# Kernel optimization log

Hardware: AMD Instinct MI355X
Metric: run time of the kernel (lower is better)

## Reference

```python
import math
import jax, jax.numpy as jnp
import numpy as np

B, N, D = 4, 4096, 1024
H = 16
DK = D // H  # 64
M = 256      # nb_features
EPS = 1e-6


def _gorf(key, n_rows, n_cols):
    """Gaussian orthogonal random matrix (n_rows, n_cols), stacked orthonormal
    blocks with chi-distributed row lengths (Performer GORF)."""
    blocks, rows_left = [], n_rows
    while rows_left > 0:
        br = min(n_cols, rows_left)
        key, k1, k2 = jax.random.split(key, 3)
        u = jax.random.normal(k1, (n_cols, n_cols), dtype=jnp.float32)
        q, r = jnp.linalg.qr(u)
        q = q * jnp.sign(jnp.diagonal(r))[None, :]  # q @ diag(sign(diag(r)))
        g = jax.random.normal(k2, (br, n_cols), dtype=jnp.float32)
        lengths = jnp.linalg.norm(g, axis=1, keepdims=True)
        blocks.append(q[:br] * lengths)
        rows_left -= br
    return jnp.concatenate(blocks, axis=0)


def setup_inputs() -> dict:
    key = jax.random.key(0)
    ks = jax.random.split(key, 8)
    x = jax.random.normal(ks[0], (B, N, D), dtype=jnp.float32)
    # True = PAD
    key_padding_mask = jax.random.randint(ks[1], (B, N), 0, 2).astype(jnp.bool_)
    # Linear params (xavier-scale init; exact scheme irrelevant to the math)
    Wqkv = jax.random.normal(ks[2], (3 * D, D), dtype=jnp.float32) * 0.02
    bqkv = jnp.zeros((3 * D,), dtype=jnp.float32)
    Wout = jax.random.normal(ks[3], (D, D), dtype=jnp.float32) * 0.02
    bout = jnp.zeros((D,), dtype=jnp.float32)
    # Per-head GORF omega, scaled by sqrt(dk) as in _draw_features
    omega = jnp.stack(
        [_gorf(jax.random.fold_in(ks[4], h), M, DK) for h in range(H)], axis=0
    ) * math.sqrt(DK)  # (H, M, dk)
    return {"x": x, "key_padding_mask": key_padding_mask, "Wqkv": Wqkv,
            "bqkv": bqkv, "Wout": Wout, "bout": bout, "omega": omega}


def _phi_exp(t, omega):
    # t: (B,H,N,dk) -> (B,H,N,M)
    proj = jnp.einsum('bhnd,hmd->bhnm', t, omega)
    sq_norm = 0.5 * jnp.sum(t * t, axis=-1, keepdims=True)
    z = proj - sq_norm
    z = z - jnp.max(z, axis=-1, keepdims=True)          # stabilize
    return jnp.exp(z) / math.sqrt(M + 1e-6)


def reference(x, key_padding_mask, Wqkv, bqkv, Wout, bout, omega):
    qkv = x @ Wqkv.T + bqkv                              # (B,N,3D)
    Q, K, V = jnp.split(qkv, 3, axis=-1)
    split = lambda t: t.reshape(B, N, H, DK).transpose(0, 2, 1, 3)  # (B,H,N,dk)
    Q, K, V = split(Q), split(K), split(V)
    valid_bool = ~key_padding_mask                       # (B,N), True=real token
    valid = valid_bool[:, None, :, None].astype(x.dtype) # (B,1,N,1)
    Qp = _phi_exp(Q, omega)                              # (B,H,N,M)
    Kp = _phi_exp(K, omega) * valid                      # zero PAD keys
    KV = jnp.einsum('bhnm,bhnd->bhmd', Kp, V)            # (B,H,M,dk)
    ksum = jnp.sum(Kp, axis=2)                           # (B,H,M)
    num = jnp.einsum('bhnm,bhmd->bhnd', Qp, KV)          # (B,H,N,dk)
    den = jnp.einsum('bhnm,bhm->bhn', Qp, ksum)[..., None] + EPS
    ctx = num / den                                      # (B,H,N,dk)
    out = ctx.transpose(0, 2, 1, 3).reshape(B, N, D)     # merge heads
    out = out @ Wout.T + bout
    out = out * valid_bool[..., None].astype(out.dtype)  # PAD queries -> exact 0
    return out
```

## Files before the change

### kernel.cpp

```cpp
#include <hip/hip_runtime.h>
#include <hip/hip_bf16.h>
#include <math.h>

#define B_  4
#define N_  4096
#define D_  1024
#define H_  16
#define DK_ 64
#define M_  256
#define R_  (B_*N_)
#define EPS_ 1e-6f
#define VTROWS_ 80
#define KVROWS_ 128
#define PHK_PAD 68
#define PHQ_PAD 264

typedef __bf16 bf16;
typedef __bf16 bf16x4 __attribute__((ext_vector_type(4)));
typedef __bf16 bf16x8 __attribute__((ext_vector_type(8)));
typedef _Float16 f16;
typedef _Float16 f16x4 __attribute__((ext_vector_type(4)));
typedef _Float16 f16x8 __attribute__((ext_vector_type(8)));
typedef float  f32x4  __attribute__((ext_vector_type(4)));

#define GLD(gp, lp) __builtin_amdgcn_global_load_lds( \
    (const __attribute__((address_space(1))) void*)(gp), \
    (__attribute__((address_space(3))) void*)(lp), 16, 0, 0)

#define BAR_()   __builtin_amdgcn_s_barrier()
#define SBAR_()  __builtin_amdgcn_sched_barrier(0)
#define PRIO1_() __builtin_amdgcn_s_setprio(1)
#define PRIO0_() __builtin_amdgcn_s_setprio(0)

__global__ __launch_bounds__(256)
void split_f16v(const float* __restrict__ in, f16* __restrict__ hi,
                f16* __restrict__ lo, int n4)
{
    int i = blockIdx.x * 256 + threadIdx.x;
    if (i < n4) {
        float4 v = ((const float4*)in)[i];
        f16x4 h = { (f16)v.x, (f16)v.y, (f16)v.z, (f16)v.w };
        ((f16x4*)hi)[i] = h;
        if (lo) {
            f16x4 l = { (f16)(v.x - (float)h[0]), (f16)(v.y - (float)h[1]),
                        (f16)(v.z - (float)h[2]), (f16)(v.w - (float)h[3]) };
            ((f16x4*)lo)[i] = l;
        }
    }
}

__global__ __launch_bounds__(256)
void f32_to_bf16v(const float* __restrict__ in, bf16* __restrict__ o, int n4)
{
    int i = blockIdx.x * 256 + threadIdx.x;
    if (i < n4) {
        float4 v = ((const float4*)in)[i];
        bf16x4 h = { (bf16)v.x, (bf16)v.y, (bf16)v.z, (bf16)v.w };
        ((bf16x4*)o)[i] = h;
    }
}

__global__ __launch_bounds__(256)
void zero_f32(float* __restrict__ p, int n)
{
    int i = blockIdx.x * 256 + threadIdx.x;
    if (i < n) p[i] = 0.f;
}

__global__ __launch_bounds__(256)
void init_vt(bf16* __restrict__ VT)
{
    int i = blockIdx.x * 256 + threadIdx.x;
    if (i >= B_*H_*16*N_) return;
    int bh  = i >> 16;
    int rem = i & 65535;
    int row = 64 + (rem >> 12);
    int n   = rem & (N_-1);
    VT[((size_t)bh*VTROWS_ + row)*N_ + n] = (row == 64) ? (bf16)1.0f : (bf16)0.0f;
}

__global__ __launch_bounds__(256)
void pack_kv(const float* __restrict__ KVt32, bf16* __restrict__ KVb)
{
    int i = blockIdx.x * 256 + threadIdx.x;
    if (i >= B_*H_*KVROWS_*M_) return;
    int bh  = i >> 15;
    int rem = i & 32767;
    int row = rem >> 8;
    int m   = rem & (M_-1);
    bf16 o = (bf16)0.0f;
    if (row < 64) {
        o = (bf16)KVt32[((size_t)bh*VTROWS_ + row)*M_ + m];
    } else if (row == 64) {
        o = (bf16)KVt32[((size_t)bh*VTROWS_ + 64)*M_ + m];
    } else if (row == 65) {
        float v = KVt32[((size_t)bh*VTROWS_ + 64)*M_ + m];
        o = (bf16)(v - (float)(bf16)v);
    }
    KVb[i] = o;
}


#define STAGE_(dstbuf, srcp, kt, half) do { \
    _Pragma("unroll") \
    for (int q_ = 0; q_ < 2; ++q_) { \
        int idx_ = q_*512 + tid; \
        int row_ = idx_ >> 3; \
        int seg_ = (idx_ & 7) ^ (row_ & 7); \
        GLD((srcp) + (size_t)((half)*128 + row_) * D_ + (kt)*64 + seg_*8, \
            &(dstbuf)[(half)*8192 + idx_*8]); \
    } } while (0)

#define LDA_(buf, i0) do { \
    _Pragma("unroll") \
    for (int i_ = 0; i_ < 4; ++i_) { \
        _Pragma("unroll") \
        for (int k_ = 0; k_ < 2; ++k_) { \
            int row_ = warp_m*128 + ((i0)+i_)*16 + m16; \
            int off_ = (row_*128 + k_*64 + quad*16) ^ ((row_ & 7) << 4); \
            a[i_][k_] = *(const f16x8*)((const char*)(buf) + off_); \
        } } } while (0)

#define LDB_(buf, j0) do { \
    _Pragma("unroll") \
    for (int j_ = 0; j_ < 2; ++j_) { \
        _Pragma("unroll") \
        for (int k_ = 0; k_ < 2; ++k_) { \
            int row_ = warp_n*64 + ((j0)+j_)*16 + m16; \
            int off_ = (row_*128 + k_*64 + quad*16) ^ ((row_ & 7) << 4); \
            b[(j0)+j_][k_] = *(const f16x8*)((const char*)(buf) + off_); \
        } } } while (0)

#define MFMA_Q(I0, J0) do { \
    _Pragma("unroll") \
    for (int i_ = 0; i_ < 4; ++i_) { \
        _Pragma("unroll") \
        for (int j_ = 0; j_ < 2; ++j_) { \
            _Pragma("unroll") \
            for (int k_ = 0; k_ < 2; ++k_) \
                acc[(I0)+i_][(J0)+j_] = __builtin_amdgcn_mfma_f32_16x16x32_f16( \
                    a[i_][k_], b[(J0)+j_][k_], acc[(I0)+i_][(J0)+j_], 0, 0, 0); \
        } } } while (0)

#define LGK0_()  do { asm volatile("s_waitcnt lgkmcnt(0)"); SBAR_(); } while (0)
#define LGK8_()  asm volatile("s_waitcnt lgkmcnt(8)")
#define VMC4_()  do { asm volatile("s_waitcnt vmcnt(4)"); SBAR_(); } while (0)

__global__ __launch_bounds__(512, 1)
void gemm_qkv(const f16* __restrict__ X, const f16* __restrict__ Wh,
              const float* __restrict__ bqkv,
              f16* __restrict__ Qh, f16* __restrict__ Kh, bf16* __restrict__ VT)
{
    __shared__ __align__(16) f16 sA[2][256*64];
    __shared__ __align__(16) f16 sB[2][256*64];
    const int tid = threadIdx.x;

    const int nwg  = gridDim.x * gridDim.y;
    int flat = blockIdx.y * gridDim.x + blockIdx.x;
    int wgid = (flat & 7) * (nwg >> 3) + (flat >> 3);
    const int bm = (wgid / 12) * 256;
    const int bn = (wgid % 12) * 256;

    const int lane = tid & 63, wave = tid >> 6;
    const int warp_m = wave >> 2, warp_n = wave & 3;
    const int m16 = lane & 15, quad = lane >> 4;

    const f16* gA = X  + (size_t)bm * D_;
    const f16* gB = Wh + (size_t)bn * D_;

    f32x4 acc[8][4];
    #pragma unroll
    for (int i = 0; i < 8; ++i)
        #pragma unroll
        for (int j = 0; j < 4; ++j)
            acc[i][j] = (f32x4){0.f, 0.f, 0.f, 0.f};

    f16x8 a[4][2], b[4][2];

    STAGE_(sA[0], gA, 0, 0);
    STAGE_(sA[0], gA, 0, 1);
    STAGE_(sB[0], gB, 0, 0);
    STAGE_(sB[0], gB, 0, 1);
    STAGE_(sB[1], gB, 1, 0);
    STAGE_(sB[1], gB, 1, 1);
    VMC4_();
    BAR_();

    for (int it = 0; it < 8; ++it) {
        const int t1 = 2*it + 1, t2 = 2*it + 2, t3 = 2*it + 3;
        LDA_(sA[0], 0); LDB_(sB[0], 0);
        STAGE_(sA[1], gA, t1, 0);
        LGK8_();
        BAR_(); LGK0_();
        PRIO1_(); MFMA_Q(0, 0); PRIO0_();
        BAR_();

        LDB_(sB[0], 2);
        STAGE_(sA[1], gA, t1, 1);
        BAR_(); LGK0_();
        PRIO1_(); MFMA_Q(0, 2); PRIO0_();
        BAR_();

        LDA_(sA[0], 4);
        if (t2 < 16) STAGE_(sB[0], gB, t2, 0);
        BAR_(); LGK0_();
        PRIO1_(); MFMA_Q(4, 2); PRIO0_();
        BAR_();

        if (t2 < 16) STAGE_(sB[0], gB, t2, 1);
        VMC4_();
        BAR_();
        PRIO1_(); MFMA_Q(4, 0); PRIO0_();
        BAR_();

        LDA_(sA[1], 0); LDB_(sB[1], 0);
        if (t2 < 16) STAGE_(sA[0], gA, t2, 0);
        LGK8_();
        BAR_(); LGK0_();
        PRIO1_(); MFMA_Q(0, 0); PRIO0_();
        BAR_();

        LDB_(sB[1], 2);
        if (t2 < 16) STAGE_(sA[0], gA, t2, 1);
        BAR_(); LGK0_();
        PRIO1_(); MFMA_Q(0, 2); PRIO0_();
        BAR_();

        LDA_(sA[1], 4);
        if (t3 < 16) STAGE_(sB[1], gB, t3, 0);
        BAR_(); LGK0_();
        PRIO1_(); MFMA_Q(4, 2); PRIO0_();
        BAR_();

        if (t3 < 16) STAGE_(sB[1], gB, t3, 1);
        VMC4_();
        BAR_();
        PRIO1_(); MFMA_Q(4, 0); PRIO0_();
        BAR_();
    }

    #pragma unroll
    for (int j = 0; j < 4; ++j) {
        int gcol = bn + warp_n*64 + j*16 + m16;
        float bv = bqkv[gcol];
        #pragma unroll
        for (int i = 0; i < 8; ++i) {
            int row0 = bm + warp_m*128 + i*16 + quad*4;
            if (gcol >= 2*D_) {
                int vcol = gcol - 2*D_;
                int hh = vcol >> 6, dd = vcol & 63;
                int bb = row0 >> 12, nn = row0 & (N_-1);
                bf16x4 pk = { (bf16)(acc[i][j][0]+bv), (bf16)(acc[i][j][1]+bv),
                              (bf16)(acc[i][j][2]+bv), (bf16)(acc[i][j][3]+bv) };
                *(bf16x4*)&VT[(((size_t)bb*H_+hh)*VTROWS_ + dd)*N_ + nn] = pk;
            } else if (gcol >= D_) {
                #pragma unroll
                for (int r = 0; r < 4; ++r)
                    Kh[(size_t)(row0+r) * D_ + gcol - D_] = (f16)(acc[i][j][r] + bv);
            } else {
                #pragma unroll
                for (int r = 0; r < 4; ++r)
                    Qh[(size_t)(row0+r) * D_ + gcol] = (f16)(acc[i][j][r] + bv);
            }
        }
    }
}

#define STAGEK_(sub_, bi_) do { \
    const int n0_ = nsp*1024 + (sub_)*128; \
    _Pragma("unroll") \
    for (int it_ = 0; it_ < 2; ++it_) { \
        int idx_ = it_*512 + tid; \
        int row_ = idx_ >> 3, seg_ = (idx_ & 7) ^ (row_ & 7); \
        GLD(Kh + (size_t)(b*N_ + n0_ + row_) * D_ + h*DK_ + seg_*8, \
            &sK[bi_][idx_*8]); \
    } } while (0)

#define STAGEVT_(sub_) do { \
    const int n0_ = nsp*1024 + (sub_)*128; \
    _Pragma("unroll") \
    for (int it_ = 0; it_ < 2; ++it_) { \
        int idx_ = it_*512 + tid; \
        int row_ = idx_ >> 4, seg_ = (idx_ & 15) ^ (row_ & 7); \
        GLD(VT + ((size_t)bh*VTROWS_ + row_)*N_ + n0_ + seg_*8, \
            &sVT[idx_*8]); \
    } \
    if (tid < 256) { \
        int idx_ = 1024 + tid; \
        int row_ = idx_ >> 4, seg_ = (idx_ & 15) ^ (row_ & 7); \
        GLD(VT + ((size_t)bh*VTROWS_ + row_)*N_ + n0_ + seg_*8, \
            &sVT[idx_*8]); \
    } } while (0)

#define STAGEOM_(arr_, src_) do { \
    _Pragma("unroll") \
    for (int q_ = 0; q_ < 4; ++q_) { \
        int idx_ = q_*512 + tid; \
        int row_ = idx_ >> 3, seg_ = (idx_ & 7) ^ (row_ & 7); \
        GLD((src_) + (size_t)row_*DK_ + seg_*8, &(arr_)[idx_*8]); \
    } } while (0)

__global__ __launch_bounds__(512, 1)
void fused_kv(const f16* __restrict__ Kh, const bf16* __restrict__ VT,
              const f16* __restrict__ omhi, const f16* __restrict__ omlo,
              const int* __restrict__ mask, float* __restrict__ KVt32)
{
    __shared__ __align__(16) f16  sK[2][128*64];
    __shared__ __align__(16) bf16 sVT[VTROWS_*128];
    __shared__ __align__(16) f16  sOmH[M_*DK_];
    __shared__ __align__(16) f16  sOmL[M_*DK_];
    __shared__ __align__(16) bf16 sPhi[M_*PHK_PAD];
    const int nsp = blockIdx.x;
    const int h = blockIdx.y, b = blockIdx.z;
    const int bh = b*H_ + h;
    const int tid = threadIdx.x, lane = tid & 63, wave = tid >> 6;
    const int m16 = lane & 15, quad = lane >> 4;
    const int wm = wave * 32;
    const int nloc = wave*16 + quad*4;
    const float inv_sqrt_m = rsqrtf((float)M_ + 1e-6f);
    const f16* omh = omhi + (size_t)h * M_ * DK_;
    const f16* oml = omlo + (size_t)h * M_ * DK_;

    f32x4 kvacc[5][2];
    #pragma unroll
    for (int d = 0; d < 5; ++d)
        #pragma unroll
        for (int j = 0; j < 2; ++j)
            kvacc[d][j] = (f32x4){0.f, 0.f, 0.f, 0.f};

    STAGEOM_(sOmH, omh);
    STAGEOM_(sOmL, oml);
    STAGEK_(0, 0);

    for (int sub = 0; sub < 8; ++sub) {
        const int cur = sub & 1;
        const int n0 = nsp*1024 + sub*128;

        asm volatile("s_waitcnt vmcnt(0) lgkmcnt(0)");
        SBAR_();
        BAR_();

        int4 mv4 = *(const int4*)&mask[b*N_ + n0 + nloc];
        const int* mv = (const int*)&mv4;
        STAGEVT_(sub);
        if (sub < 7) STAGEK_(sub+1, cur^1);

        const char* kb = (const char*)&sK[cur][0];
        const int rowb = wave*16 + m16;
        f16x8 ah0 = *(const f16x8*)(kb + ((rowb*128 +      quad*16) ^ ((rowb & 7) << 4)));
        f16x8 ah1 = *(const f16x8*)(kb + ((rowb*128 + 64 + quad*16) ^ ((rowb & 7) << 4)));

        f32x4 acc[16];
        #pragma unroll
        for (int j = 0; j < 16; ++j) acc[j] = (f32x4){0.f, 0.f, 0.f, 0.f};

        PRIO1_();
        #pragma unroll
        for (int j = 0; j < 16; ++j) {
            int rowm = j*16 + m16;
            int bo0 = (rowm*128 +      quad*16) ^ ((rowm & 7) << 4);
            int bo1 = (rowm*128 + 64 + quad*16) ^ ((rowm & 7) << 4);
            f16x8 bh0 = *(const f16x8*)((const char*)sOmH + bo0);
            f16x8 bh1 = *(const f16x8*)((const char*)sOmH + bo1);
            f16x8 bl0 = *(const f16x8*)((const char*)sOmL + bo0);
            f16x8 bl1 = *(const f16x8*)((const char*)sOmL + bo1);
            acc[j] = __builtin_amdgcn_mfma_f32_16x16x32_f16(ah0, bh0, acc[j], 0,0,0);
            acc[j] = __builtin_amdgcn_mfma_f32_16x16x32_f16(ah0, bl0, acc[j], 0,0,0);
            acc[j] = __builtin_amdgcn_mfma_f32_16x16x32_f16(ah1, bh1, acc[j], 0,0,0);
            acc[j] = __builtin_amdgcn_mfma_f32_16x16x32_f16(ah1, bl1, acc[j], 0,0,0);
        }
        PRIO0_();

        #pragma unroll
        for (int r = 0; r < 4; ++r) {
            float mx = acc[0][r];
            #pragma unroll
            for (int j = 1; j < 16; ++j) mx = fmaxf(mx, acc[j][r]);
            mx = fmaxf(mx, __shfl_xor(mx, 1, 64));
            mx = fmaxf(mx, __shfl_xor(mx, 2, 64));
            mx = fmaxf(mx, __shfl_xor(mx, 4, 64));
            mx = fmaxf(mx, __shfl_xor(mx, 8, 64));
            #pragma unroll
            for (int j = 0; j < 16; ++j)
                acc[j][r] = __expf(acc[j][r] - mx) * inv_sqrt_m;
        }

        if (wave < 4) {
            #pragma unroll
            for (int j = 0; j < 16; ++j) {
                bf16x4 pk;
                #pragma unroll
                for (int r = 0; r < 4; ++r)
                    pk[r] = mv[r] ? (bf16)0.0f : (bf16)acc[j][r];
                *(bf16x4*)&sPhi[(j*16 + m16)*PHK_PAD + nloc] = pk;
            }
        }
        asm volatile("s_waitcnt lgkmcnt(0)");
        if (sub < 7) { asm volatile("s_waitcnt vmcnt(2)"); }
        else         { asm volatile("s_waitcnt vmcnt(0)"); }
        SBAR_();
        BAR_();

        PRIO1_();
        #pragma unroll
        for (int ks = 0; ks < 2; ++ks) {
            bf16x8 av[5], bp[2];
            #pragma unroll
            for (int d = 0; d < 5; ++d) {
                int rowv = d*16 + m16;
                av[d] = *(const bf16x8*)((const char*)sVT +
                        ((rowv*256 + ks*64 + quad*16) ^ ((rowv & 7) << 4)));
            }
            #pragma unroll
            for (int j = 0; j < 2; ++j)
                bp[j] = *(const bf16x8*)&sPhi[(wm + j*16 + m16)*PHK_PAD + ks*32 + quad*8];
            #pragma unroll
            for (int d = 0; d < 5; ++d)
                #pragma unroll
                for (int j = 0; j < 2; ++j)
                    kvacc[d][j] = __builtin_amdgcn_mfma_f32_16x16x32_bf16(
                        av[d], bp[j], kvacc[d][j], 0, 0, 0);
        }
        PRIO0_();
        asm volatile("s_waitcnt lgkmcnt(0)");
        SBAR_();
        BAR_();

        if (wave >= 4) {
            #pragma unroll
            for (int j = 0; j < 16; ++j) {
                bf16x4 pk;
                #pragma unroll
                for (int r = 0; r < 4; ++r)
                    pk[r] = mv[r] ? (bf16)0.0f : (bf16)acc[j][r];
                *(bf16x4*)&sPhi[(j*16 + m16)*PHK_PAD + (nloc - 64)] = pk;
            }
        }
        asm volatile("s_waitcnt lgkmcnt(0)");
        SBAR_();
        BAR_();

        PRIO1_();
        #pragma unroll
        for (int ks = 0; ks < 2; ++ks) {
            bf16x8 av[5], bp[2];
            #pragma unroll
            for (int d = 0; d < 5; ++d) {
                int rowv = d*16 + m16;
                av[d] = *(const bf16x8*)((const char*)sVT +
                        ((rowv*256 + 128 + ks*64 + quad*16) ^ ((rowv & 7) << 4)));
            }
            #pragma unroll
            for (int j = 0; j < 2; ++j)
                bp[j] = *(const bf16x8*)&sPhi[(wm + j*16 + m16)*PHK_PAD + ks*32 + quad*8];
            #pragma unroll
            for (int d = 0; d < 5; ++d)
                #pragma unroll
                for (int j = 0; j < 2; ++j)
                    kvacc[d][j] = __builtin_amdgcn_mfma_f32_16x16x32_bf16(
                        av[d], bp[j], kvacc[d][j], 0, 0, 0);
        }
        PRIO0_();
    }

    #pragma unroll
    for (int d = 0; d < 5; ++d)
        #pragma unroll
        for (int j = 0; j < 2; ++j) {
            int drow = d*16 + quad*4;
            int m = wm + j*16 + m16;
            #pragma unroll
            for (int r = 0; r < 4; ++r)
                atomicAdd(&KVt32[((size_t)bh*VTROWS_ + drow + r)*M_ + m],
                          kvacc[d][j][r]);
        }
}

__global__ __launch_bounds__(512, 1)
void fused_ctx(const f16* __restrict__ Qh, const f16* __restrict__ omhi,
               const f16* __restrict__ omlo, const bf16* __restrict__ KVb,
               bf16* __restrict__ ctx)
{
    __shared__ __align__(16) f16  sOmH[M_*DK_];
    __shared__ __align__(16) f16  sOmL[M_*DK_];
    __shared__ __align__(16) bf16 sPhi[128*PHQ_PAD];
    __shared__ float sden[2][128];
    const int nsp = blockIdx.x;
    const int h = blockIdx.y, b = blockIdx.z;
    const int bh = b*H_ + h;
    const int tid = threadIdx.x, lane = tid & 63, wave = tid >> 6;
    const int m16 = lane & 15, quad = lane >> 4;
    const float inv_sqrt_m = rsqrtf((float)M_ + 1e-6f);
    const f16* omh = omhi + (size_t)h * M_ * DK_;
    const f16* oml = omlo + (size_t)h * M_ * DK_;

    STAGEOM_(sOmH, omh);
    STAGEOM_(sOmL, oml);
    asm volatile("s_waitcnt vmcnt(0)");
    SBAR_();
    BAR_();

    const int wq = wave >> 2;
    const int wc = wave & 3;

    for (int nb = 0; nb < 8; ++nb) {
        const int q0 = nsp*1024 + nb*128;

        const int rowq = wave*16 + m16;
        f16x8 ah0 = *(const f16x8*)&Qh[(size_t)(b*N_ + q0 + rowq)*D_ + h*DK_ + quad*8];
        f16x8 ah1 = *(const f16x8*)&Qh[(size_t)(b*N_ + q0 + rowq)*D_ + h*DK_ + 32 + quad*8];

        f32x4 acc[16];
        #pragma unroll
        for (int j = 0; j < 16; ++j) acc[j] = (f32x4){0.f, 0.f, 0.f, 0.f};

        PRIO1_();
        #pragma unroll
        for (int j = 0; j < 16; ++j) {
            int rowm = j*16 + m16;
            int bo0 = (rowm*128 +      quad*16) ^ ((rowm & 7) << 4);
            int bo1 = (rowm*128 + 64 + quad*16) ^ ((rowm & 7) << 4);
            f16x8 bh0 = *(const f16x8*)((const char*)sOmH + bo0);
            f16x8 bh1 = *(const f16x8*)((const char*)sOmH + bo1);
            f16x8 bl0 = *(const f16x8*)((const char*)sOmL + bo0);
            f16x8 bl1 = *(const f16x8*)((const char*)sOmL + bo1);
            acc[j] = __builtin_amdgcn_mfma_f32_16x16x32_f16(ah0, bh0, acc[j], 0,0,0);
            acc[j] = __builtin_amdgcn_mfma_f32_16x16x32_f16(ah0, bl0, acc[j], 0,0,0);
            acc[j] = __builtin_amdgcn_mfma_f32_16x16x32_f16(ah1, bh1, acc[j], 0,0,0);
            acc[j] = __builtin_amdgcn_mfma_f32_16x16x32_f16(ah1, bl1, acc[j], 0,0,0);
        }
        PRIO0_();

        bf16x8 wf[2][8];
        #pragma unroll
        for (int jr = 0; jr < 2; ++jr) {
            int rowk = wc*32 + jr*16 + m16;
            #pragma unroll
            for (int ks = 0; ks < 8; ++ks)
                wf[jr][ks] = *(const bf16x8*)&KVb[((size_t)bh*KVROWS_ + rowk)*M_
                                                  + ks*32 + quad*8];
        }

        #pragma unroll
        for (int r = 0; r < 4; ++r) {
            float mx = acc[0][r];
            #pragma unroll
            for (int j = 1; j < 16; ++j) mx = fmaxf(mx, acc[j][r]);
            mx = fmaxf(mx, __shfl_xor(mx, 1, 64));
            mx = fmaxf(mx, __shfl_xor(mx, 2, 64));
            mx = fmaxf(mx, __shfl_xor(mx, 4, 64));
            mx = fmaxf(mx, __shfl_xor(mx, 8, 64));
            #pragma unroll
            for (int j = 0; j < 16; ++j)
                acc[j][r] = __expf(acc[j][r] - mx) * inv_sqrt_m;
        }

        {
            int nloc0 = wave*16 + quad*4;
            #pragma unroll
            for (int j = 0; j < 16; ++j)
                #pragma unroll
                for (int r = 0; r < 4; ++r)
                    sPhi[(nloc0 + r)*PHQ_PAD + j*16 + m16] = (bf16)acc[j][r];
        }
        asm volatile("s_waitcnt lgkmcnt(0)");
        SBAR_();
        BAR_();

        f32x4 cacc[4][2];
        #pragma unroll
        for (int i = 0; i < 4; ++i)
            #pragma unroll
            for (int j = 0; j < 2; ++j)
                cacc[i][j] = (f32x4){0.f, 0.f, 0.f, 0.f};

        PRIO1_();
        #pragma unroll
        for (int ks = 0; ks < 8; ++ks) {
            bf16x8 af[4];
            #pragma unroll
            for (int i = 0; i < 4; ++i)
                af[i] = *(const bf16x8*)&sPhi[(wq*64 + i*16 + m16)*PHQ_PAD
                                              + ks*32 + quad*8];
            #pragma unroll
            for (int i = 0; i < 4; ++i)
                #pragma unroll
                for (int jr = 0; jr < 2; ++jr)
                    cacc[i][jr] = __builtin_amdgcn_mfma_f32_16x16x32_bf16(
                        af[i], wf[jr][ks], cacc[i][jr], 0, 0, 0);
        }
        PRIO0_();

        if (wc == 2 && m16 < 2) {
            #pragma unroll
            for (int i = 0; i < 4; ++i)
                #pragma unroll
                for (int r = 0; r < 4; ++r)
                    sden[m16][wq*64 + i*16 + quad*4 + r] = cacc[i][0][r];
        }
        asm volatile("s_waitcnt lgkmcnt(0)");
        SBAR_();
        BAR_();

        if (wc < 2) {
            #pragma unroll
            for (int i = 0; i < 4; ++i) {
                #pragma unroll
                for (int r = 0; r < 4; ++r) {
                    int lrow = wq*64 + i*16 + quad*4 + r;
                    float den = sden[0][lrow] + sden[1][lrow] + EPS_;
                    #pragma unroll
                    for (int jr = 0; jr < 2; ++jr)
                        ctx[(size_t)(b*N_ + q0 + lrow)*D_ + h*DK_
                            + wc*32 + jr*16 + m16] = (bf16)(cacc[i][jr][r] / den);
                }
            }
        }
        asm volatile("s_waitcnt lgkmcnt(0)");
        SBAR_();
        BAR_();
    }
}

__global__ __launch_bounds__(256)
void gemm_out(const bf16* __restrict__ A, const bf16* __restrict__ W,
              const float* __restrict__ bias, float* __restrict__ C,
              const int* __restrict__ mask)
{
    __shared__ bf16 sA[128*64];
    __shared__ bf16 sB[128*64];
    const int tid  = threadIdx.x;
    const int bm   = blockIdx.y * 128;
    const int bn   = blockIdx.x * 128;
    const int lane = tid & 63, wave = tid >> 6;
    const int wm   = (wave & 1) * 64, wn = (wave >> 1) * 64;
    const int m16  = lane & 15, quad = lane >> 4;

    f32x4 acc[4][4];
    #pragma unroll
    for (int i = 0; i < 4; ++i)
        #pragma unroll
        for (int j = 0; j < 4; ++j)
            acc[i][j] = (f32x4){0.f, 0.f, 0.f, 0.f};

    for (int k0 = 0; k0 < D_; k0 += 64) {
        __syncthreads();
        #pragma unroll
        for (int it = 0; it < 4; ++it) {
            int idx = it*256 + tid;
            int row = idx >> 3, seg = idx & 7;
            GLD(A + (size_t)(bm + row) * D_ + k0 + seg*8, &sA[idx*8]);
            GLD(W + (size_t)(bn + row) * D_ + k0 + seg*8, &sB[idx*8]);
        }
        __syncthreads();
        #pragma unroll
        for (int kk = 0; kk < 64; kk += 32) {
            bf16x8 af[4], bfr[4];
            #pragma unroll
            for (int i = 0; i < 4; ++i)
                af[i] = *(const bf16x8*)&sA[(wm + i*16 + m16)*64 + kk + quad*8];
            #pragma unroll
            for (int j = 0; j < 4; ++j)
                bfr[j] = *(const bf16x8*)&sB[(wn + j*16 + m16)*64 + kk + quad*8];
            #pragma unroll
            for (int i = 0; i < 4; ++i)
                #pragma unroll
                for (int j = 0; j < 4; ++j)
                    acc[i][j] = __builtin_amdgcn_mfma_f32_16x16x32_bf16(
                        af[i], bfr[j], acc[i][j], 0, 0, 0);
        }
    }

    #pragma unroll
    for (int j = 0; j < 4; ++j) {
        int col = bn + wn + j*16 + m16;
        float bv = bias[col];
        #pragma unroll
        for (int i = 0; i < 4; ++i) {
            int row0 = bm + wm + i*16 + quad*4;
            #pragma unroll
            for (int r = 0; r < 4; ++r) {
                int row = row0 + r;
                float v = acc[i][j][r] + bv;
                if (mask[row] != 0) v = 0.0f;
                C[(size_t)row * D_ + col] = v;
            }
        }
    }
}

extern "C" void kernel_launch(void* const* d_in, const int* in_sizes, int n_in,
                              void* d_out, int out_size, void* d_ws, size_t ws_size,
                              hipStream_t stream)
{
    const float* x     = (const float*)d_in[0];
    const int*   mask  = (const int*)d_in[1];
    const float* Wqkv  = (const float*)d_in[2];
    const float* bqkv  = (const float*)d_in[3];
    const float* Wout  = (const float*)d_in[4];
    const float* bout  = (const float*)d_in[5];
    const float* omega = (const float*)d_in[6];
    float* out = (float*)d_out;

    char* w = (char*)d_ws;
    f16*   Wh    = (f16*)w;    w += (size_t)3*D_*D_ * 2;
    bf16*  Wob   = (bf16*)w;   w += (size_t)D_*D_ * 2;
    f16*   omhi  = (f16*)w;    w += (size_t)H_*M_*DK_ * 2;
    f16*   omlo  = (f16*)w;    w += (size_t)H_*M_*DK_ * 2;
    f16*   xh    = (f16*)w;    w += (size_t)R_ * D_ * 2;
    f16*   Qh    = (f16*)w;    w += (size_t)R_ * D_ * 2;
    f16*   Kh    = (f16*)w;    w += (size_t)R_ * D_ * 2;
    bf16*  VT    = (bf16*)w;   w += (size_t)B_*H_*VTROWS_*N_ * 2;
    float* KVt32 = (float*)w;  w += (size_t)B_*H_*VTROWS_*M_ * 4;
    bf16*  KVb   = (bf16*)w;   w += (size_t)B_*H_*KVROWS_*M_ * 2;
    bf16*  VC    = (bf16*)Kh;

    split_f16v<<<(R_*D_/4 + 255)/256, 256, 0, stream>>>(x, xh, nullptr, R_*D_/4);
    split_f16v<<<(3*D_*D_/4 + 255)/256, 256, 0, stream>>>(Wqkv, Wh, nullptr, 3*D_*D_/4);
    split_f16v<<<(H_*M_*DK_/4 + 255)/256, 256, 0, stream>>>(omega, omhi, omlo, H_*M_*DK_/4);
    f32_to_bf16v<<<(D_*D_/4 + 255)/256, 256, 0, stream>>>(Wout, Wob, D_*D_/4);
    zero_f32<<<(B_*H_*VTROWS_*M_ + 255)/256, 256, 0, stream>>>(KVt32, B_*H_*VTROWS_*M_);
    init_vt<<<(B_*H_*16*N_ + 255)/256, 256, 0, stream>>>(VT);

    gemm_qkv<<<dim3(3*D_/256, R_/256), 512, 0, stream>>>(xh, Wh, bqkv, Qh, Kh, VT);

    fused_kv<<<dim3(4, H_, B_), 512, 0, stream>>>(Kh, VT, omhi, omlo, mask, KVt32);

    pack_kv<<<(B_*H_*KVROWS_*M_ + 255)/256, 256, 0, stream>>>(KVt32, KVb);

    fused_ctx<<<dim3(4, H_, B_), 512, 0, stream>>>(Qh, omhi, omlo, KVb, VC);

    gemm_out<<<dim3(8, R_/128), 256, 0, stream>>>(VC, Wob, bout, out, mask);
}
```

Baseline: 457.5 us.

## Split QKV GEMM into QK and V kernels; reuse pipelined 256x256 GEMM for output projection

The fused QKV GEMM is split into two kernels. The Q/K kernel swaps the MFMA operands so each lane holds four consecutive columns and writes vectorized f16x4 row-major stores instead of scalar stores. The V kernel keeps the transposed bf16 layout. The output projection moves from a simple 128x128 single-buffered kernel to the same 8-phase double-buffered 256x256 pipeline with vectorized float4 stores. The cost is one more launch and a smaller output grid (256 blocks), which may leave some compute units idle.

```diff
diff --git a/kernel.cpp b/kernel.cpp
--- a/kernel.cpp
+++ b/kernel.cpp
@@ -31,6 +31,9 @@
 #define SBAR_()  __builtin_amdgcn_sched_barrier(0)
 #define PRIO1_() __builtin_amdgcn_s_setprio(1)
 #define PRIO0_() __builtin_amdgcn_s_setprio(0)
+#define LGK0_()  do { asm volatile("s_waitcnt lgkmcnt(0)"); SBAR_(); } while (0)
+#define LGK8_()  asm volatile("s_waitcnt lgkmcnt(8)")
+#define VMC4_()  do { asm volatile("s_waitcnt vmcnt(4)"); SBAR_(); } while (0)
 
 __global__ __launch_bounds__(256)
 void split_f16v(const float* __restrict__ in, f16* __restrict__ hi,
@@ -100,7 +103,6 @@
     KVb[i] = o;
 }
 
-
 #define STAGE_(dstbuf, srcp, kt, half) do { \
     _Pragma("unroll") \
     for (int q_ = 0; q_ < 2; ++q_) { \
@@ -111,55 +113,129 @@
             &(dstbuf)[(half)*8192 + idx_*8]); \
     } } while (0)
 
-#define LDA_(buf, i0) do { \
+#define LDA_G(T, buf, i0) do { \
     _Pragma("unroll") \
     for (int i_ = 0; i_ < 4; ++i_) { \
         _Pragma("unroll") \
         for (int k_ = 0; k_ < 2; ++k_) { \
             int row_ = warp_m*128 + ((i0)+i_)*16 + m16; \
             int off_ = (row_*128 + k_*64 + quad*16) ^ ((row_ & 7) << 4); \
-            a[i_][k_] = *(const f16x8*)((const char*)(buf) + off_); \
+            a[i_][k_] = *(const T*)((const char*)(buf) + off_); \
         } } } while (0)
 
-#define LDB_(buf, j0) do { \
+#define LDB_G(T, buf, j0) do { \
     _Pragma("unroll") \
     for (int j_ = 0; j_ < 2; ++j_) { \
         _Pragma("unroll") \
         for (int k_ = 0; k_ < 2; ++k_) { \
             int row_ = warp_n*64 + ((j0)+j_)*16 + m16; \
             int off_ = (row_*128 + k_*64 + quad*16) ^ ((row_ & 7) << 4); \
-            b[(j0)+j_][k_] = *(const f16x8*)((const char*)(buf) + off_); \
+            b[(j0)+j_][k_] = *(const T*)((const char*)(buf) + off_); \
         } } } while (0)
 
-#define MFMA_Q(I0, J0) do { \
-    _Pragma("unroll") \
-    for (int i_ = 0; i_ < 4; ++i_) { \
+#define MFMA_F16N(I0, J0) do { \
+    _Pragma("unroll") \
+    for (int i_ = 0; i_ < 4; ++i_) \
         _Pragma("unroll") \
-        for (int j_ = 0; j_ < 2; ++j_) { \
+        for (int j_ = 0; j_ < 2; ++j_) \
             _Pragma("unroll") \
             for (int k_ = 0; k_ < 2; ++k_) \
                 acc[(I0)+i_][(J0)+j_] = __builtin_amdgcn_mfma_f32_16x16x32_f16( \
                     a[i_][k_], b[(J0)+j_][k_], acc[(I0)+i_][(J0)+j_], 0, 0, 0); \
-        } } } while (0)
-
-#define LGK0_()  do { asm volatile("s_waitcnt lgkmcnt(0)"); SBAR_(); } while (0)
-#define LGK8_()  asm volatile("s_waitcnt lgkmcnt(8)")
-#define VMC4_()  do { asm volatile("s_waitcnt vmcnt(4)"); SBAR_(); } while (0)
-
-__global__ __launch_bounds__(512, 1)
-void gemm_qkv(const f16* __restrict__ X, const f16* __restrict__ Wh,
-              const float* __restrict__ bqkv,
-              f16* __restrict__ Qh, f16* __restrict__ Kh, bf16* __restrict__ VT)
+    } while (0)
+
+#define MFMA_F16S(I0, J0) do { \
+    _Pragma("unroll") \
+    for (int i_ = 0; i_ < 4; ++i_) \
+        _Pragma("unroll") \
+        for (int j_ = 0; j_ < 2; ++j_) \
+            _Pragma("unroll") \
+            for (int k_ = 0; k_ < 2; ++k_) \
+                acc[(I0)+i_][(J0)+j_] = __builtin_amdgcn_mfma_f32_16x16x32_f16( \
+                    b[(J0)+j_][k_], a[i_][k_], acc[(I0)+i_][(J0)+j_], 0, 0, 0); \
+    } while (0)
+
+#define MFMA_BF16S(I0, J0) do { \
+    _Pragma("unroll") \
+    for (int i_ = 0; i_ < 4; ++i_) \
+        _Pragma("unroll") \
+        for (int j_ = 0; j_ < 2; ++j_) \
+            _Pragma("unroll") \
+            for (int k_ = 0; k_ < 2; ++k_) \
+                acc[(I0)+i_][(J0)+j_] = __builtin_amdgcn_mfma_f32_16x16x32_bf16( \
+                    b[(J0)+j_][k_], a[i_][k_], acc[(I0)+i_][(J0)+j_], 0, 0, 0); \
+    } while (0)
+
+#define KLOOP_8PH(MFMA_OP) \
+    STAGE_(sA[0], gA, 0, 0); \
+    STAGE_(sA[0], gA, 0, 1); \
+    STAGE_(sB[0], gB, 0, 0); \
+    STAGE_(sB[0], gB, 0, 1); \
+    STAGE_(sB[1], gB, 1, 0); \
+    STAGE_(sB[1], gB, 1, 1); \
+    VMC4_(); \
+    BAR_(); \
+    for (int it = 0; it < 8; ++it) { \
+        const int t1 = 2*it + 1, t2 = 2*it + 2, t3 = 2*it + 3; \
+        LDA_G(FRAG_T, sA[0], 0); LDB_G(FRAG_T, sB[0], 0); \
+        STAGE_(sA[1], gA, t1, 0); \
+        LGK8_(); \
+        BAR_(); LGK0_(); \
+        PRIO1_(); MFMA_OP(0, 0); PRIO0_(); \
+        BAR_(); \
+        LDB_G(FRAG_T, sB[0], 2); \
+        STAGE_(sA[1], gA, t1, 1); \
+        BAR_(); LGK0_(); \
+        PRIO1_(); MFMA_OP(0, 2); PRIO0_(); \
+        BAR_(); \
+        LDA_G(FRAG_T, sA[0], 4); \
+        if (t2 < 16) STAGE_(sB[0], gB, t2, 0); \
+        BAR_(); LGK0_(); \
+        PRIO1_(); MFMA_OP(4, 2); PRIO0_(); \
+        BAR_(); \
+        if (t2 < 16) STAGE_(sB[0], gB, t2, 1); \
+        VMC4_(); \
+        BAR_(); \
+        PRIO1_(); MFMA_OP(4, 0); PRIO0_(); \
+        BAR_(); \
+        LDA_G(FRAG_T, sA[1], 0); LDB_G(FRAG_T, sB[1], 0); \
+        if (t2 < 16) STAGE_(sA[0], gA, t2, 0); \
+        LGK8_(); \
+        BAR_(); LGK0_(); \
+        PRIO1_(); MFMA_OP(0, 0); PRIO0_(); \
+        BAR_(); \
+        LDB_G(FRAG_T, sB[1], 2); \
+        if (t2 < 16) STAGE_(sA[0], gA, t2, 1); \
+        BAR_(); LGK0_(); \
+        PRIO1_(); MFMA_OP(0, 2); PRIO0_(); \
+        BAR_(); \
+        LDA_G(FRAG_T, sA[1], 4); \
+        if (t3 < 16) STAGE_(sB[1], gB, t3, 0); \
+        BAR_(); LGK0_(); \
+        PRIO1_(); MFMA_OP(4, 2); PRIO0_(); \
+        BAR_(); \
+        if (t3 < 16) STAGE_(sB[1], gB, t3, 1); \
+        VMC4_(); \
+        BAR_(); \
+        PRIO1_(); MFMA_OP(4, 0); PRIO0_(); \
+        BAR_(); \
+    }
+
+#define FRAG_T f16x8
+__global__ __launch_bounds__(512)
+void gemm_qkv_qk(const f16* __restrict__ X, const f16* __restrict__ Wh,
+                 const float* __restrict__ bqkv,
+                 f16* __restrict__ Qh, f16* __restrict__ Kh)
 {
     __shared__ __align__(16) f16 sA[2][256*64];
     __shared__ __align__(16) f16 sB[2][256*64];
     const int tid = threadIdx.x;
 
-    const int nwg  = gridDim.x * gridDim.y;
+    const int nwg = gridDim.x * gridDim.y;
     int flat = blockIdx.y * gridDim.x + blockIdx.x;
     int wgid = (flat & 7) * (nwg >> 3) + (flat >> 3);
-    const int bm = (wgid / 12) * 256;
-    const int bn = (wgid % 12) * 256;
+    const int bm = (wgid >> 3) * 256;
+    const int bn = (wgid & 7) * 256;
 
     const int lane = tid & 63, wave = tid >> 6;
     const int warp_m = wave >> 2, warp_n = wave & 3;
@@ -174,97 +250,128 @@
         #pragma unroll
         for (int j = 0; j < 4; ++j)
             acc[i][j] = (f32x4){0.f, 0.f, 0.f, 0.f};
-
     f16x8 a[4][2], b[4][2];
 
-    STAGE_(sA[0], gA, 0, 0);
-    STAGE_(sA[0], gA, 0, 1);
-    STAGE_(sB[0], gB, 0, 0);
-    STAGE_(sB[0], gB, 0, 1);
-    STAGE_(sB[1], gB, 1, 0);
-    STAGE_(sB[1], gB, 1, 1);
-    VMC4_();
-    BAR_();
-
-    for (int it = 0; it < 8; ++it) {
-        const int t1 = 2*it + 1, t2 = 2*it + 2, t3 = 2*it + 3;
-        LDA_(sA[0], 0); LDB_(sB[0], 0);
-        STAGE_(sA[1], gA, t1, 0);
-        LGK8_();
-        BAR_(); LGK0_();
-        PRIO1_(); MFMA_Q(0, 0); PRIO0_();
-        BAR_();
-
-        LDB_(sB[0], 2);
-        STAGE_(sA[1], gA, t1, 1);
-        BAR_(); LGK0_();
-        PRIO1_(); MFMA_Q(0, 2); PRIO0_();
-        BAR_();
-
-        LDA_(sA[0], 4);
-        if (t2 < 16) STAGE_(sB[0], gB, t2, 0);
-        BAR_(); LGK0_();
-        PRIO1_(); MFMA_Q(4, 2); PRIO0_();
-        BAR_();
-
-        if (t2 < 16) STAGE_(sB[0], gB, t2, 1);
-        VMC4_();
-        BAR_();
-        PRIO1_(); MFMA_Q(4, 0); PRIO0_();
-        BAR_();
-
-        LDA_(sA[1], 0); LDB_(sB[1], 0);
-        if (t2 < 16) STAGE_(sA[0], gA, t2, 0);
-        LGK8_();
-        BAR_(); LGK0_();
-        PRIO1_(); MFMA_Q(0, 0); PRIO0_();
-        BAR_();
-
-        LDB_(sB[1], 2);
-        if (t2 < 16) STAGE_(sA[0], gA, t2, 1);
-        BAR_(); LGK0_();
-        PRIO1_(); MFMA_Q(0, 2); PRIO0_();
-        BAR_();
-
-        LDA_(sA[1], 4);
-        if (t3 < 16) STAGE_(sB[1], gB, t3, 0);
-        BAR_(); LGK0_();
-        PRIO1_(); MFMA_Q(4, 2); PRIO0_();
-        BAR_();
-
-        if (t3 < 16) STAGE_(sB[1], gB, t3, 1);
-        VMC4_();
-        BAR_();
-        PRIO1_(); MFMA_Q(4, 0); PRIO0_();
-        BAR_();
-    }
+    KLOOP_8PH(MFMA_F16S)
+
+    f16* outp = (bn >= D_) ? Kh : Qh;
+    const int cofs = (bn >= D_) ? D_ : 0;
+    #pragma unroll
+    for (int j = 0; j < 4; ++j) {
+        int gcol0 = bn + warp_n*64 + j*16 + quad*4;
+        float4 bv = *(const float4*)&bqkv[gcol0];
+        int col0 = gcol0 - cofs;
+        #pragma unroll
+        for (int i = 0; i < 8; ++i) {
+            int row = bm + warp_m*128 + i*16 + m16;
+            f16x4 pk = { (f16)(acc[i][j][0] + bv.x), (f16)(acc[i][j][1] + bv.y),
+                         (f16)(acc[i][j][2] + bv.z), (f16)(acc[i][j][3] + bv.w) };
+            *(f16x4*)&outp[(size_t)row * D_ + col0] = pk;
+        }
+    }
+}
+
+__global__ __launch_bounds__(512)
+void gemm_qkv_v(const f16* __restrict__ X, const f16* __restrict__ Wh,
+                const float* __restrict__ bqkv, bf16* __restrict__ VT)
+{
+    __shared__ __align__(16) f16 sA[2][256*64];
+    __shared__ __align__(16) f16 sB[2][256*64];
+    const int tid = threadIdx.x;
+
+    const int nwg = gridDim.x * gridDim.y;
+    int flat = blockIdx.y * gridDim.x + blockIdx.x;
+    int wgid = (flat & 7) * (nwg >> 3) + (flat >> 3);
+    const int bm = (wgid >> 2) * 256;
+    const int bn = 2*D_ + (wgid & 3) * 256;
+
+    const int lane = tid & 63, wave = tid >> 6;
+    const int warp_m = wave >> 2, warp_n = wave & 3;
+    const int m16 = lane & 15, quad = lane >> 4;
+
+    const f16* gA = X  + (size_t)bm * D_;
+    const f16* gB = Wh + (size_t)bn * D_;
+
+    f32x4 acc[8][4];
+    #pragma unroll
+    for (int i = 0; i < 8; ++i)
+        #pragma unroll
+        for (int j = 0; j < 4; ++j)
+            acc[i][j] = (f32x4){0.f, 0.f, 0.f, 0.f};
+    f16x8 a[4][2], b[4][2];
+
+    KLOOP_8PH(MFMA_F16N)
 
     #pragma unroll
     for (int j = 0; j < 4; ++j) {
         int gcol = bn + warp_n*64 + j*16 + m16;
         float bv = bqkv[gcol];
+        int vcol = gcol - 2*D_;
+        int hh = vcol >> 6, dd = vcol & 63;
         #pragma unroll
         for (int i = 0; i < 8; ++i) {
             int row0 = bm + warp_m*128 + i*16 + quad*4;
-            if (gcol >= 2*D_) {
-                int vcol = gcol - 2*D_;
-                int hh = vcol >> 6, dd = vcol & 63;
-                int bb = row0 >> 12, nn = row0 & (N_-1);
-                bf16x4 pk = { (bf16)(acc[i][j][0]+bv), (bf16)(acc[i][j][1]+bv),
-                              (bf16)(acc[i][j][2]+bv), (bf16)(acc[i][j][3]+bv) };
-                *(bf16x4*)&VT[(((size_t)bb*H_+hh)*VTROWS_ + dd)*N_ + nn] = pk;
-            } else if (gcol >= D_) {
-                #pragma unroll
-                for (int r = 0; r < 4; ++r)
-                    Kh[(size_t)(row0+r) * D_ + gcol - D_] = (f16)(acc[i][j][r] + bv);
+            int bb = row0 >> 12, nn = row0 & (N_-1);
+            bf16x4 pk = { (bf16)(acc[i][j][0]+bv), (bf16)(acc[i][j][1]+bv),
+                          (bf16)(acc[i][j][2]+bv), (bf16)(acc[i][j][3]+bv) };
+            *(bf16x4*)&VT[(((size_t)bb*H_+hh)*VTROWS_ + dd)*N_ + nn] = pk;
+        }
+    }
+}
+#undef FRAG_T
+
+#define FRAG_T bf16x8
+__global__ __launch_bounds__(512)
+void gemm_out8(const bf16* __restrict__ A, const bf16* __restrict__ W,
+               const float* __restrict__ bias, float* __restrict__ C,
+               const int* __restrict__ mask)
+{
+    __shared__ __align__(16) bf16 sA[2][256*64];
+    __shared__ __align__(16) bf16 sB[2][256*64];
+    const int tid = threadIdx.x;
+
+    const int nwg = gridDim.x * gridDim.y;
+    int flat = blockIdx.y * gridDim.x + blockIdx.x;
+    int wgid = (flat & 7) * (nwg >> 3) + (flat >> 3);
+    const int bm = (wgid >> 2) * 256;
+    const int bn = (wgid & 3) * 256;
+
+    const int lane = tid & 63, wave = tid >> 6;
+    const int warp_m = wave >> 2, warp_n = wave & 3;
+    const int m16 = lane & 15, quad = lane >> 4;
+
+    const bf16* gA = A + (size_t)bm * D_;
+    const bf16* gB = W + (size_t)bn * D_;
+
+    f32x4 acc[8][4];
+    #pragma unroll
+    for (int i = 0; i < 8; ++i)
+        #pragma unroll
+        for (int j = 0; j < 4; ++j)
+            acc[i][j] = (f32x4){0.f, 0.f, 0.f, 0.f};
+    bf16x8 a[4][2], b[4][2];
+
+    KLOOP_8PH(MFMA_BF16S)
+
+    #pragma unroll
+    for (int j = 0; j < 4; ++j) {
+        int col0 = bn + warp_n*64 + j*16 + quad*4;
+        float4 bv = *(const float4*)&bias[col0];
+        #pragma unroll
+        for (int i = 0; i < 8; ++i) {
+            int row = bm + warp_m*128 + i*16 + m16;
+            float4 v;
+            if (mask[row] != 0) {
+                v = make_float4(0.f, 0.f, 0.f, 0.f);
             } else {
-                #pragma unroll
-                for (int r = 0; r < 4; ++r)
-                    Qh[(size_t)(row0+r) * D_ + gcol] = (f16)(acc[i][j][r] + bv);
+                v = make_float4(acc[i][j][0] + bv.x, acc[i][j][1] + bv.y,
+                                acc[i][j][2] + bv.z, acc[i][j][3] + bv.w);
             }
-        }
-    }
-}
+            *(float4*)&C[(size_t)row * D_ + col0] = v;
+        }
+    }
+}
+#undef FRAG_T
 
 #define STAGEK_(sub_, bi_) do { \
     const int n0_ = nsp*1024 + (sub_)*128; \
@@ -622,73 +729,6 @@
     }
 }
 
-__global__ __launch_bounds__(256)
-void gemm_out(const bf16* __restrict__ A, const bf16* __restrict__ W,
-              const float* __restrict__ bias, float* __restrict__ C,
-              const int* __restrict__ mask)
-{
-    __shared__ bf16 sA[128*64];
-    __shared__ bf16 sB[128*64];
-    const int tid  = threadIdx.x;
-    const int bm   = blockIdx.y * 128;
-    const int bn   = blockIdx.x * 128;
-    const int lane = tid & 63, wave = tid >> 6;
-    const int wm   = (wave & 1) * 64, wn = (wave >> 1) * 64;
-    const int m16  = lane & 15, quad = lane >> 4;
-
-    f32x4 acc[4][4];
-    #pragma unroll
-    for (int i = 0; i < 4; ++i)
-        #pragma unroll
-        for (int j = 0; j < 4; ++j)
-            acc[i][j] = (f32x4){0.f, 0.f, 0.f, 0.f};
-
-    for (int k0 = 0; k0 < D_; k0 += 64) {
-        __syncthreads();
-        #pragma unroll
-        for (int it = 0; it < 4; ++it) {
-            int idx = it*256 + tid;
-            int row = idx >> 3, seg = idx & 7;
-            GLD(A + (size_t)(bm + row) * D_ + k0 + seg*8, &sA[idx*8]);
-            GLD(W + (size_t)(bn + row) * D_ + k0 + seg*8, &sB[idx*8]);
-        }
-        __syncthreads();
-        #pragma unroll
-        for (int kk = 0; kk < 64; kk += 32) {
-            bf16x8 af[4], bfr[4];
-            #pragma unroll
-            for (int i = 0; i < 4; ++i)
-                af[i] = *(const bf16x8*)&sA[(wm + i*16 + m16)*64 + kk + quad*8];
-            #pragma unroll
-            for (int j = 0; j < 4; ++j)
-                bfr[j] = *(const bf16x8*)&sB[(wn + j*16 + m16)*64 + kk + quad*8];
-            #pragma unroll
-            for (int i = 0; i < 4; ++i)
-                #pragma unroll
-                for (int j = 0; j < 4; ++j)
-                    acc[i][j] = __builtin_amdgcn_mfma_f32_16x16x32_bf16(
-                        af[i], bfr[j], acc[i][j], 0, 0, 0);
-        }
-    }
-
-    #pragma unroll
-    for (int j = 0; j < 4; ++j) {
-        int col = bn + wn + j*16 + m16;
-        float bv = bias[col];
-        #pragma unroll
-        for (int i = 0; i < 4; ++i) {
-            int row0 = bm + wm + i*16 + quad*4;
-            #pragma unroll
-            for (int r = 0; r < 4; ++r) {
-                int row = row0 + r;
-                float v = acc[i][j][r] + bv;
-                if (mask[row] != 0) v = 0.0f;
-                C[(size_t)row * D_ + col] = v;
-            }
-        }
-    }
-}
-
 extern "C" void kernel_launch(void* const* d_in, const int* in_sizes, int n_in,
                               void* d_out, int out_size, void* d_ws, size_t ws_size,
                               hipStream_t stream)
@@ -722,7 +762,8 @@
     zero_f32<<<(B_*H_*VTROWS_*M_ + 255)/256, 256, 0, stream>>>(KVt32, B_*H_*VTROWS_*M_);
     init_vt<<<(B_*H_*16*N_ + 255)/256, 256, 0, stream>>>(VT);
 
-    gemm_qkv<<<dim3(3*D_/256, R_/256), 512, 0, stream>>>(xh, Wh, bqkv, Qh, Kh, VT);
+    gemm_qkv_qk<<<dim3(8, R_/256), 512, 0, stream>>>(xh, Wh, bqkv, Qh, Kh);
+    gemm_qkv_v <<<dim3(4, R_/256), 512, 0, stream>>>(xh, Wh, bqkv, VT);
 
     fused_kv<<<dim3(4, H_, B_), 512, 0, stream>>>(Kh, VT, omhi, omlo, mask, KVt32);
 
@@ -730,5 +771,5 @@
 
     fused_ctx<<<dim3(4, H_, B_), 512, 0, stream>>>(Qh, omhi, omlo, KVb, VC);
 
-    gemm_out<<<dim3(8, R_/128), 256, 0, stream>>>(VC, Wob, bout, out, mask);
-}
+    gemm_out8<<<dim3(4, R_/256), 512, 0, stream>>>(VC, Wob, bout, out, mask);
+}
```

New measurement: 438.9 us. 1.04x faster.
